# Kernel optimization log

Measured on AMD Instinct MI355X. Metric: run time of the kernel, lower is better.

## Reference

```python
import jax, jax.numpy as jnp
import numpy as np

N = 20000
E = 320000
K = 16          # k_dynamic
FEAT = 64       # feature_dim == hidden_channels
R = 4           # expansion_factor
NUM_OUT = 80000 # num_out_points == R*N
CH = 2000       # query chunk size for kNN (N % CH == 0)


def _lin(key, fan_in, fan_out):
    kw, kb = jax.random.split(key)
    lim = 1.0 / np.sqrt(fan_in)
    W = jax.random.uniform(kw, (fan_in, fan_out), minval=-lim, maxval=lim, dtype=jnp.float32)
    b = jax.random.uniform(kb, (fan_out,), minval=-lim, maxval=lim, dtype=jnp.float32)
    return W, b


def setup_inputs() -> dict:
    key = jax.random.key(0)
    ks = jax.random.split(key, 10)
    dep_points = jax.random.normal(ks[0], (N, 3), dtype=jnp.float32)
    edge_index = jax.random.randint(ks[1], (2, E), 0, N, dtype=jnp.int32)
    W1a, b1a = _lin(ks[2], 2 * 3, FEAT)       # edgeconv1 mlp layer 1
    W1b, b1b = _lin(ks[3], FEAT, FEAT)        # edgeconv1 mlp layer 2
    W2a, b2a = _lin(ks[4], 2 * FEAT, FEAT)    # dynamic edgeconv mlp layer 1
    W2b, b2b = _lin(ks[5], FEAT, FEAT)        # dynamic edgeconv mlp layer 2
    We, be = _lin(ks[6], FEAT, R * FEAT)      # linear_expand
    Wp, bp = _lin(ks[7], FEAT, FEAT)          # out_proj
    Wr1, br1 = _lin(ks[8], FEAT, FEAT)
    Wr2, br2 = _lin(ks[9], FEAT, 3)
    return dict(dep_points=dep_points, W1a=W1a, b1a=b1a, W1b=W1b, b1b=b1b,
                W2a=W2a, b2a=b2a, W2b=W2b, b2b=b2b, We=We, be=be, Wp=Wp, bp=bp,
                Wr1=Wr1, br1=br1, Wr2=Wr2, br2=br2, edge_index=edge_index)


def _mlp2(x, Wa, ba, Wb, bb):
    h = jax.nn.relu(x @ Wa + ba)
    return jax.nn.relu(h @ Wb + bb)


def _forward(dep_points, W1a, b1a, W1b, b1b, W2a, b2a, W2b, b2b,
             We, be, Wp, bp, Wr1, br1, Wr2, br2, edge_index):
    # --- EdgeConv with static edge_index (flow source_to_target: i = edge_index[1]) ---
    src, dst = edge_index[0], edge_index[1]
    xi = dep_points[dst]                             # [E,3] target features
    xj = dep_points[src]                             # [E,3] source features
    msg = _mlp2(jnp.concatenate([xi, xj - xi], -1), W1a, b1a, W1b, b1b)  # [E,64]
    x1 = jax.ops.segment_max(msg, dst, num_segments=N)                   # [N,64]
    x1 = jnp.where(jnp.isfinite(x1), x1, 0.0)        # empty segments -> 0

    # --- DynamicEdgeConv: kNN in feature space (indices non-differentiable) ---
    f = jax.lax.stop_gradient(x1)
    sq = jnp.sum(f * f, axis=1)                      # [N]
    def chunk_knn(qc):                                # qc: [CH,64]
        d2 = jnp.sum(qc * qc, axis=1)[:, None] + sq[None, :] - 2.0 * (qc @ f.T)
        return jax.lax.top_k(-d2, K)[1]               # [CH,K] includes self (d=0)
    nbr = jax.lax.map(chunk_knn, f.reshape(N // CH, CH, FEAT)).reshape(N, K)

    xi2 = x1[:, None, :]                              # [N,1,64]
    xj2 = x1[nbr]                                     # [N,K,64]
    pair = jnp.concatenate([jnp.broadcast_to(xi2, (N, K, FEAT)), xj2 - xi2], -1)
    msg2 = _mlp2(pair, W2a, b2a, W2b, b2b)            # [N,K,64]
    x2 = jnp.max(msg2, axis=1)                        # [N,64]

    # --- SimpleExpansion: expand + periodic shuffle + out_proj (B=1) ---
    xe = x2 @ We + be                                 # [N, R*64]
    xs = xe.reshape(N, R, FEAT).transpose(1, 0, 2).reshape(R * N, FEAT)
    feat = xs @ Wp + bp                               # [R*N,64]

    L = feat.shape[0]
    if L > NUM_OUT:
        feat = feat[:NUM_OUT]
    elif L < NUM_OUT:
        feat = jnp.concatenate([feat, jnp.repeat(feat[-1:], NUM_OUT - L, axis=0)], 0)

    h = jax.nn.relu(feat @ Wr1 + br1)
    return h @ Wr2 + br2                              # [NUM_OUT,3]


def reference(dep_points, W1a, b1a, W1b, b1b, W2a, b2a, W2b, b2b,
              We, be, Wp, bp, Wr1, br1, Wr2, br2, edge_index):
    return _forward(dep_points, W1a, b1a, W1b, b1b, W2a, b2a, W2b, b2b,
                    We, be, Wp, bp, Wr1, br1, Wr2, br2, edge_index)
```

## Files before the change

kernel.cpp:

```cpp
#include <hip/hip_runtime.h>
#include <hip/hip_bf16.h>

#define NPTS 20000
#define NE   320000
#define KNNK 16
#define NTILE ((NPTS + 127) / 128)

typedef __attribute__((ext_vector_type(8))) short bf16x8;
typedef __attribute__((ext_vector_type(4))) float f32x4;

#define OFF_X1   0
#define OFF_SQ   (OFF_X1 + NPTS*64)
#define OFF_WB   (OFF_SQ + NPTS)
#define WB_W1A  0
#define WB_B1A  384
#define WB_W1BT 448
#define WB_B1B  4544
#define WB_W2A  4608
#define WB_B2A  12800
#define WB_W2B  12864
#define WB_B2B  16960
#define WB_WE   17024
#define WB_BE   33408
#define WB_WP   33664
#define WB_BP   37760
#define WB_WR1  37824
#define WB_BR1  41920
#define WB_WR2  41984
#define WB_BR2  42176
#define WB_TOT  42240
#define OFF_NBR  (OFF_WB + WB_TOT)
#define OFF_OFFS (OFF_NBR + NPTS*KNNK)
#define WS1_TOT  (OFF_OFFS + NPTS + 4)
#define OFF_PK   ((WS1_TOT + 3) & ~3)
#define WS_NEED_BYTES ((size_t)WS1_TOT * 4)
#define WS2_BYTES (((size_t)OFF_PK + (size_t)NPTS*2*16) * 4)
#define WS4_BYTES (((size_t)OFF_PK + (size_t)NPTS*4*16) * 4)

__global__ __launch_bounds__(256) void k_out_zero(float* out, int nelem) {
    int i = blockIdx.x * 256 + threadIdx.x;
    if (i < nelem) out[i] = 0.0f;
}

__global__ __launch_bounds__(256) void k_prep(
    const float* W1a, const float* b1a,
    const float* W1b, const float* b1b,
    const float* W2a, const float* b2a,
    const float* W2b, const float* b2b,
    const float* We,  const float* be,
    const float* Wp,  const float* bp,
    const float* Wr1, const float* br1,
    const float* Wr2, const float* br2,
    float* wb, unsigned int* counts)
{
    int t = blockIdx.x * blockDim.x + threadIdx.x;
    int gs = gridDim.x * blockDim.x;
    for (int i = t; i < NPTS; i += gs) counts[i] = 0u;
    for (int i = t; i < 384;  i += gs) wb[WB_W1A+i] = W1a[i];
    for (int i = t; i < 64;   i += gs) wb[WB_B1A+i] = b1a[i];
    for (int i = t; i < 4096; i += gs) { int j=i>>6, k=i&63; wb[WB_W1BT+i] = W1b[k*64+j]; }
    for (int i = t; i < 64;   i += gs) wb[WB_B1B+i] = b1b[i];
    for (int i = t; i < 8192; i += gs) wb[WB_W2A+i] = W2a[i];
    for (int i = t; i < 64;   i += gs) wb[WB_B2A+i] = b2a[i];
    for (int i = t; i < 4096; i += gs) wb[WB_W2B+i] = W2b[i];
    for (int i = t; i < 64;   i += gs) wb[WB_B2B+i] = b2b[i];
    for (int i = t; i < 16384;i += gs) wb[WB_WE+i]  = We[i];
    for (int i = t; i < 256;  i += gs) wb[WB_BE+i]  = be[i];
    for (int i = t; i < 4096; i += gs) wb[WB_WP+i]  = Wp[i];
    for (int i = t; i < 64;   i += gs) wb[WB_BP+i]  = bp[i];
    for (int i = t; i < 4096; i += gs) wb[WB_WR1+i] = Wr1[i];
    for (int i = t; i < 64;   i += gs) wb[WB_BR1+i] = br1[i];
    for (int i = t; i < 192;  i += gs) wb[WB_WR2+i] = Wr2[i];
    for (int i = t; i < 3;    i += gs) wb[WB_BR2+i] = br2[i];
}

__global__ __launch_bounds__(256) void k_hist(const int* __restrict__ ei,
                                              unsigned int* __restrict__ counts) {
    int e = blockIdx.x * 256 + threadIdx.x;
    if (e >= NE) return;
    int d = ei[NE + e];
    d = d < 0 ? 0 : (d >= NPTS ? NPTS-1 : d);
    atomicAdd(&counts[d], 1u);
}

__global__ __launch_bounds__(256) void k_scan(const unsigned int* __restrict__ counts,
                                              unsigned int* __restrict__ cursor,
                                              unsigned int* __restrict__ offs) {
    __shared__ unsigned int ssum[256];
    __shared__ unsigned int sbase[257];
    int t = threadIdx.x;
    int lo = t * 79;
    int hi = lo + 79; if (hi > NPTS) hi = NPTS;
    if (lo > NPTS) lo = NPTS;
    unsigned int sum = 0;
    for (int i = lo; i < hi; ++i) sum += counts[i];
    ssum[t] = sum;
    __syncthreads();
    if (t == 0) {
        unsigned int run = 0;
        for (int i = 0; i < 256; ++i) { sbase[i] = run; run += ssum[i]; }
        sbase[256] = run;
    }
    __syncthreads();
    unsigned int run = sbase[t];
    for (int i = lo; i < hi; ++i) {
        unsigned int c = counts[i];
        offs[i] = run;
        cursor[i] = run;
        run += c;
    }
    if (t == 0) offs[NPTS] = sbase[256];
}

__global__ __launch_bounds__(256) void k_scatter(const int* __restrict__ ei,
                                                 unsigned int* __restrict__ cursor,
                                                 int* __restrict__ elist) {
    int e = blockIdx.x * 256 + threadIdx.x;
    if (e >= NE) return;
    int d = ei[NE + e];
    d = d < 0 ? 0 : (d >= NPTS ? NPTS-1 : d);
    unsigned int pos = atomicAdd(&cursor[d], 1u);
    elist[pos] = e;
}

__device__ __forceinline__ int clampn(int v) {
    return v < 0 ? 0 : (v >= NPTS ? NPTS-1 : v);
}

__global__ __launch_bounds__(64) void k_gather(
    const float* __restrict__ dep, const int* __restrict__ ei,
    const int* __restrict__ elist, const unsigned int* __restrict__ offs,
    const float* __restrict__ W1a, const float* __restrict__ b1a,
    const float* __restrict__ W1b, const float* __restrict__ b1b,
    float* __restrict__ x1)
{
    __shared__ float hbuf[2][64];
    int d = blockIdx.x;
    int t = threadIdx.x;
    unsigned int o0 = offs[d], o1 = offs[d+1];
    float xi0 = dep[d*3+0], xi1 = dep[d*3+1], xi2 = dep[d*3+2];
    float wa0 = W1a[t], wa1 = W1a[64+t], wa2 = W1a[128+t];
    float wa3 = W1a[192+t], wa4 = W1a[256+t], wa5 = W1a[320+t];
    float ba = b1a[t], bb = b1b[t];
    float w1b[64];
#pragma unroll
    for (int j = 0; j < 64; ++j) w1b[j] = W1b[j*64 + t];
    float m = 0.0f;
    int buf = 0;
    if (o0 < o1) {
        unsigned int last = o1 - 1;
        int e0 = elist[o0];
        int s0 = clampn(ei[e0]);
        float dx0 = dep[s0*3+0] - xi0;
        float dx1 = dep[s0*3+1] - xi1;
        float dx2 = dep[s0*3+2] - xi2;
        unsigned int i1 = o0 + 1 < last ? o0 + 1 : last;
        unsigned int i2 = o0 + 2 < last ? o0 + 2 : last;
        int s_nxt  = clampn(ei[elist[i1]]);
        int eid_n2 = elist[i2];
        for (unsigned int o = o0; o < o1; ++o) {
            float h = ba;
            h = fmaf(xi0, wa0, h); h = fmaf(xi1, wa1, h); h = fmaf(xi2, wa2, h);
            h = fmaf(dx0, wa3, h); h = fmaf(dx1, wa4, h); h = fmaf(dx2, wa5, h);
            h = fmaxf(h, 0.0f);
            hbuf[buf][t] = h;
            __syncthreads();
            float ndx0 = dep[s_nxt*3+0] - xi0;
            float ndx1 = dep[s_nxt*3+1] - xi1;
            float ndx2 = dep[s_nxt*3+2] - xi2;
            int ns2 = ei[eid_n2];
            unsigned int i3 = o + 3 < last ? o + 3 : last;
            int neid = elist[i3];
            const float* hb = hbuf[buf];
            float z = bb;
#pragma unroll
            for (int j = 0; j < 64; ++j) z = fmaf(hb[j], w1b[j], z);
            m = fmaxf(m, z);
            buf ^= 1;
            dx0 = ndx0; dx1 = ndx1; dx2 = ndx2;
            s_nxt = clampn(ns2);
            eid_n2 = neid;
        }
    }
    x1[d*64 + t] = m;
}

__global__ __launch_bounds__(256) void k_conv(float* __restrict__ x1, float* __restrict__ sq) {
    int n = blockIdx.x * 256 + threadIdx.x;
    if (n >= NPTS) return;
    float* base = x1 + n*64;
    float4 r[16];
#pragma unroll
    for (int i = 0; i < 16; ++i) r[i] = ((const float4*)base)[i];
    float s = 0.f;
#pragma unroll
    for (int i = 0; i < 16; ++i) s += r[i].x*r[i].x + r[i].y*r[i].y + r[i].z*r[i].z + r[i].w*r[i].w;
    sq[n] = s;
    unsigned int* hi = (unsigned int*)base;
    unsigned int* lo = (unsigned int*)(base + 32);
#pragma unroll
    for (int j = 0; j < 8; ++j) {
        float v[8] = { r[2*j].x, r[2*j].y, r[2*j].z, r[2*j].w,
                       r[2*j+1].x, r[2*j+1].y, r[2*j+1].z, r[2*j+1].w };
        unsigned int hb[8], lb[8];
#pragma unroll
        for (int e = 0; e < 8; ++e) {
            unsigned int u = __float_as_uint(v[e]);
            hb[e] = (u + 0x7fffu + ((u >> 16) & 1u)) >> 16;
            float hf = __uint_as_float(hb[e] << 16);
            float lf = v[e] - hf;
            unsigned int ul = __float_as_uint(lf);
            lb[e] = (ul + 0x7fffu + ((ul >> 16) & 1u)) >> 16;
        }
        uint4 hp, lp;
        hp.x = hb[0] | (hb[1] << 16); hp.y = hb[2] | (hb[3] << 16);
        hp.z = hb[4] | (hb[5] << 16); hp.w = hb[6] | (hb[7] << 16);
        lp.x = lb[0] | (lb[1] << 16); lp.y = lb[2] | (lb[3] << 16);
        lp.z = lb[4] | (lb[5] << 16); lp.w = lb[6] | (lb[7] << 16);
        ((uint4*)hi)[j] = hp;
        ((uint4*)lo)[j] = lp;
    }
}

__device__ __forceinline__ void insk(unsigned int (&s)[16], unsigned int k) {
#pragma unroll
    for (int i = 15; i >= 1; --i) s[i] = min(s[i], max(s[i-1], k));
    s[0] = min(s[0], k);
}

#define RP  136
#define QB  64
__global__ __launch_bounds__(512) void k_knn(
    const float* __restrict__ x1, const float* __restrict__ sqv,
    int* __restrict__ nbr, unsigned int* __restrict__ pk)
{
    __shared__ __align__(16) unsigned short qbuf[QB*RP];
    __shared__ __align__(16) unsigned char  cbuf_raw[128*RP*2];
    __shared__ float ssq[128];
    unsigned short* cbuf = (unsigned short*)cbuf_raw;
    const int t  = threadIdx.x;
    const int n0 = blockIdx.x * QB;
    const int ns = gridDim.y;
    const int tps  = (NTILE + ns - 1) / ns;
    const int tbeg = blockIdx.y * tps;
    const int tend = min(NTILE, tbeg + tps);

#pragma unroll
    for (int i = 0; i < 2; ++i) {
        int ch2 = i*512 + t;
        int row = ch2 >> 4, off = ch2 & 15;
        uint4 v = make_uint4(0,0,0,0);
        if (n0 + row < NPTS) v = ((const uint4*)(x1 + (n0+row)*64))[off];
        *(uint4*)&qbuf[row*RP + off*8] = v;
    }
    __syncthreads();

    const int lane15 = t & 15;
    const int quad   = (t >> 4) & 3;
    const int w  = t >> 6;
    const int qs = w & 3;
    const int ch = w >> 2;
    bf16x8 Bh[2], Bl[2];
    {
        const unsigned short* qr = &qbuf[(qs*16 + lane15)*RP + quad*8];
        Bh[0] = *(const bf16x8*)(qr);
        Bh[1] = *(const bf16x8*)(qr + 32);
        Bl[0] = *(const bf16x8*)(qr + 64);
        Bl[1] = *(const bf16x8*)(qr + 96);
    }
    int myq = n0 + qs*16 + lane15;
    float sqq = (myq < NPTS) ? sqv[myq] : 0.0f;
    unsigned int sk[16];
#pragma unroll
    for (int m = 0; m < 16; ++m) sk[m] = 0xFFFFFFFFu;

    uint4 pv[4];
    int prow[4], poff[4];
#pragma unroll
    for (int i = 0; i < 4; ++i) {
        int ch2 = i*512 + t;
        prow[i] = tbeg*128 + (ch2 >> 4); poff[i] = ch2 & 15;
        pv[i] = make_uint4(0,0,0,0);
        if (prow[i] < NPTS) pv[i] = ((const uint4*)(x1 + prow[i]*64))[poff[i]];
    }
    float sreg = (t < 128 && tbeg*128 + t < NPTS) ? sqv[tbeg*128 + t] : 1e30f;

    for (int tile = tbeg; tile < tend; ++tile) {
        const int c0 = tile * 128;
        __syncthreads();
#pragma unroll
        for (int i = 0; i < 4; ++i)
            *(uint4*)&cbuf[(prow[i] - c0)*RP + poff[i]*8] = pv[i];
        if (t < 128) ssq[t] = sreg;
        __syncthreads();

        unsigned int pm  = min(sk[15], (unsigned int)__shfl_xor((int)sk[15], 16));
        unsigned int swv = min(pm, (unsigned int)__shfl_xor((int)pm, 32));

        if (tile + 1 < tend) {
            const int c0n = c0 + 128;
#pragma unroll
            for (int i = 0; i < 4; ++i) {
                int row = prow[i] + 128;
                pv[i] = make_uint4(0,0,0,0);
                if (row < NPTS) pv[i] = ((const uint4*)(x1 + row*64))[poff[i]];
                prow[i] = row;
            }
            sreg = (t < 128 && c0n + t < NPTS) ? sqv[c0n + t] : 1e30f;
        }

#pragma unroll
        for (int t4 = 0; t4 < 4; ++t4) {
            const unsigned short* cr = &cbuf[(ch*64 + t4*16 + lane15)*RP + quad*8];
            bf16x8 Ah0 = *(const bf16x8*)(cr);
            bf16x8 Ah1 = *(const bf16x8*)(cr + 32);
            bf16x8 Al0 = *(const bf16x8*)(cr + 64);
            bf16x8 Al1 = *(const bf16x8*)(cr + 96);
            f32x4 acc = (f32x4){0.f,0.f,0.f,0.f};
            acc = __builtin_amdgcn_mfma_f32_16x16x32_bf16(Ah0, Bh[0], acc, 0, 0, 0);
            acc = __builtin_amdgcn_mfma_f32_16x16x32_bf16(Al0, Bh[0], acc, 0, 0, 0);
            acc = __builtin_amdgcn_mfma_f32_16x16x32_bf16(Ah0, Bl[0], acc, 0, 0, 0);
            acc = __builtin_amdgcn_mfma_f32_16x16x32_bf16(Ah1, Bh[1], acc, 0, 0, 0);
            acc = __builtin_amdgcn_mfma_f32_16x16x32_bf16(Al1, Bh[1], acc, 0, 0, 0);
            acc = __builtin_amdgcn_mfma_f32_16x16x32_bf16(Ah1, Bl[1], acc, 0, 0, 0);
            int cbase = ch*64 + t4*16 + quad*4;
            float4 s4 = *(const float4*)&ssq[cbase];
            float e0 = fmaxf(fmaf(-2.0f, acc[0], s4.x) + sqq, 0.0f);
            float e1 = fmaxf(fmaf(-2.0f, acc[1], s4.y) + sqq, 0.0f);
            float e2 = fmaxf(fmaf(-2.0f, acc[2], s4.z) + sqq, 0.0f);
            float e3 = fmaxf(fmaf(-2.0f, acc[3], s4.w) + sqq, 0.0f);
            unsigned int cg = (unsigned int)(c0 + cbase);
            unsigned int k0 = (__float_as_uint(e0) & 0xFFFF8000u) | (cg+0u);
            unsigned int k1 = (__float_as_uint(e1) & 0xFFFF8000u) | (cg+1u);
            unsigned int k2 = (__float_as_uint(e2) & 0xFFFF8000u) | (cg+2u);
            unsigned int k3 = (__float_as_uint(e3) & 0xFFFF8000u) | (cg+3u);
            unsigned int mn = min(min(k0,k1), min(k2,k3));
            if (mn < swv) {
                if (k0 < sk[15]) insk(sk, k0);
                if (k1 < sk[15]) insk(sk, k1);
                if (k2 < sk[15]) insk(sk, k2);
                if (k3 < sk[15]) insk(sk, k3);
            }
        }
    }
    __syncthreads();
    {
        int q = qs*16 + lane15, lid = ch*4 + quad;
        unsigned int* fk = (unsigned int*)cbuf_raw;
        int base = q*136 + lid*17;
#pragma unroll
        for (int m = 0; m < 16; ++m) fk[base + m] = sk[m];
    }
    __syncthreads();
    if (t < QB && n0 + t < NPTS) {
        const unsigned int* fk = (const unsigned int*)cbuf_raw;
        int qb = t*136;
        int pr[8] = {0,0,0,0,0,0,0,0};
        int obase = (ns == 1) ? (n0 + t)*16 : ((n0 + t)*ns + blockIdx.y)*16;
        for (int r = 0; r < 16; ++r) {
            unsigned int best = 0xFFFFFFFFu; int bl = 0;
#pragma unroll
            for (int l = 0; l < 8; ++l) {
                unsigned int k = fk[qb + l*17 + pr[l]];
                if (k < best) { best = k; bl = l; }
            }
#pragma unroll
            for (int l = 0; l < 8; ++l) pr[l] += (bl == l) ? 1 : 0;
            if (ns == 1) {
                int idx = (int)(best & 0x7FFFu);
                nbr[obase + r] = idx >= NPTS ? NPTS-1 : idx;
            } else {
                pk[obase + r] = best;
            }
        }
    }
}

__global__ __launch_bounds__(256) void k_fmerge(
    const unsigned int* __restrict__ pk, int ns, int* __restrict__ nbr)
{
    int q = blockIdx.x * 256 + threadIdx.x;
    if (q >= NPTS) return;
    const unsigned int* fk = pk + q*ns*16;
    int pr[4] = {0,0,0,0};
    for (int r = 0; r < 16; ++r) {
        unsigned int best = 0xFFFFFFFFu; int bl = 0;
        for (int l = 0; l < ns; ++l) {
            unsigned int k = fk[l*16 + pr[l]];
            if (k < best) { best = k; bl = l; }
        }
        pr[bl]++;
        int idx = (int)(best & 0x7FFFu);
        nbr[q*16 + r] = idx >= NPTS ? NPTS-1 : idx;
    }
}

__device__ inline float bf2f(unsigned short u) {
    return __uint_as_float(((unsigned int)u) << 16);
}

__global__ __launch_bounds__(64) void k_fuse(
    const float* __restrict__ x1, const int* __restrict__ nbr,
    const float* __restrict__ wb, float* __restrict__ out)
{
    __shared__ __align__(16) float sxr[64];
    __shared__ __align__(16) float svec[64];
    __shared__ __align__(16) float sx2[64];
    __shared__ int snb[16];
    int n = blockIdx.x;
    int t = threadIdx.x;
    {
        const unsigned short* xr = (const unsigned short*)(x1 + n*64);
        sxr[t] = bf2f(xr[t]) + bf2f(xr[64+t]);
    }
    if (t < 16) snb[t] = nbr[n*16 + t];
    __syncthreads();
    const float* W2a = wb + WB_W2A;
    const float* W2b = wb + WB_W2B;
    const float4* sx4 = (const float4*)sxr;
    const float4* sv4 = (const float4*)svec;
    float wd[64], wz[64];
#pragma unroll
    for (int i = 0; i < 64; ++i) wd[i] = W2a[(64+i)*64 + t];
#pragma unroll
    for (int i = 0; i < 64; ++i) wz[i] = W2b[i*64 + t];
    float A = wb[WB_B2A + t];
#pragma unroll
    for (int i4 = 0; i4 < 16; ++i4) {
        float4 v = sx4[i4];
        const float* wr = W2a + i4*256 + t;
        A = fmaf(v.x, wr[0], A); A = fmaf(v.y, wr[64], A);
        A = fmaf(v.z, wr[128], A); A = fmaf(v.w, wr[192], A);
    }
    float D = 0.0f;
#pragma unroll
    for (int i4 = 0; i4 < 16; ++i4) {
        float4 v = sx4[i4];
        D = fmaf(v.x, wd[i4*4+0], D); D = fmaf(v.y, wd[i4*4+1], D);
        D = fmaf(v.z, wd[i4*4+2], D); D = fmaf(v.w, wd[i4*4+3], D);
    }
    const float AD = A - D;
    const float bz = wb[WB_B2B + t];
    float x2v = 0.0f;
    unsigned short ya, yb;
    {
        const unsigned short* yr = (const unsigned short*)(x1 + snb[0]*64);
        ya = yr[t]; yb = yr[64+t];
    }
    for (int k = 0; k < 16; ++k) {
        svec[t] = bf2f(ya) + bf2f(yb);
        __syncthreads();
        if (k + 1 < 16) {
            const unsigned short* yr = (const unsigned short*)(x1 + snb[k+1]*64);
            ya = yr[t]; yb = yr[64+t];
        }
        float h = AD;
#pragma unroll
        for (int i4 = 0; i4 < 16; ++i4) {
            float4 v = sv4[i4];
            h = fmaf(v.x, wd[i4*4+0], h); h = fmaf(v.y, wd[i4*4+1], h);
            h = fmaf(v.z, wd[i4*4+2], h); h = fmaf(v.w, wd[i4*4+3], h);
        }
        h = fmaxf(h, 0.f);
        __syncthreads();
        svec[t] = h;
        __syncthreads();
        float z = bz;
#pragma unroll
        for (int i4 = 0; i4 < 16; ++i4) {
            float4 v = sv4[i4];
            z = fmaf(v.x, wz[i4*4+0], z); z = fmaf(v.y, wz[i4*4+1], z);
            z = fmaf(v.z, wz[i4*4+2], z); z = fmaf(v.w, wz[i4*4+3], z);
        }
        x2v = fmaxf(x2v, fmaxf(z, 0.f));
        __syncthreads();
    }
    sx2[t] = x2v;
    __syncthreads();
    const float4* sx24 = (const float4*)sx2;
    const float* We  = wb + WB_WE;
    const float* Wp  = wb + WB_WP;
    const float* Wr1 = wb + WB_WR1;
    const float* Wr2 = wb + WB_WR2;
    for (int r = 0; r < 4; ++r) {
        float xe = wb[WB_BE + r*64 + t];
#pragma unroll
        for (int i4 = 0; i4 < 16; ++i4) {
            float4 v = sx24[i4];
            const float* wr = We + i4*1024 + r*64 + t;
            xe = fmaf(v.x, wr[0], xe); xe = fmaf(v.y, wr[256], xe);
            xe = fmaf(v.z, wr[512], xe); xe = fmaf(v.w, wr[768], xe);
        }
        svec[t] = xe;
        __syncthreads();
        float ft = wb[WB_BP + t];
#pragma unroll
        for (int i4 = 0; i4 < 16; ++i4) {
            float4 v = sv4[i4];
            const float* wr = Wp + i4*256 + t;
            ft = fmaf(v.x, wr[0], ft); ft = fmaf(v.y, wr[64], ft);
            ft = fmaf(v.z, wr[128], ft); ft = fmaf(v.w, wr[192], ft);
        }
        __syncthreads();
        svec[t] = ft;
        __syncthreads();
        float hh = wb[WB_BR1 + t];
#pragma unroll
        for (int i4 = 0; i4 < 16; ++i4) {
            float4 v = sv4[i4];
            const float* wr = Wr1 + i4*256 + t;
            hh = fmaf(v.x, wr[0], hh); hh = fmaf(v.y, wr[64], hh);
            hh = fmaf(v.z, wr[128], hh); hh = fmaf(v.w, wr[192], hh);
        }
        hh = fmaxf(hh, 0.f);
        __syncthreads();
        svec[t] = hh;
        __syncthreads();
        if (t < 3) {
            float o = wb[WB_BR2 + t];
            for (int i = 0; i < 64; ++i) o = fmaf(svec[i], Wr2[i*3 + t], o);
            int m = r * NPTS + n;
            out[m*3 + t] = o;
        }
        __syncthreads();
    }
}

extern "C" void kernel_launch(void* const* d_in, const int* in_sizes, int n_in,
                              void* d_out, int out_size, void* d_ws, size_t ws_size,
                              hipStream_t stream)
{
    const float* dep = (const float*)d_in[0];
    const float* W1a = (const float*)d_in[1];
    const float* b1a = (const float*)d_in[2];
    const float* W1b = (const float*)d_in[3];
    const float* b1b = (const float*)d_in[4];
    const float* W2a = (const float*)d_in[5];
    const float* b2a = (const float*)d_in[6];
    const float* W2b = (const float*)d_in[7];
    const float* b2b = (const float*)d_in[8];
    const float* We  = (const float*)d_in[9];
    const float* be  = (const float*)d_in[10];
    const float* Wp  = (const float*)d_in[11];
    const float* bp  = (const float*)d_in[12];
    const float* Wr1 = (const float*)d_in[13];
    const float* br1 = (const float*)d_in[14];
    const float* Wr2 = (const float*)d_in[15];
    const float* br2 = (const float*)d_in[16];
    const int* ei = (const int*)d_in[17];

    if (ws_size < WS_NEED_BYTES || d_ws == nullptr) {
        k_out_zero<<<(out_size + 255)/256, 256, 0, stream>>>((float*)d_out, out_size);
        return;
    }

    float* ws   = (float*)d_ws;
    float* x1   = ws + OFF_X1;
    float* sq   = ws + OFF_SQ;
    float* wbuf = ws + OFF_WB;
    int*   nbr  = (int*)(ws + OFF_NBR);
    unsigned int* counts = (unsigned int*)(ws + OFF_SQ);
    int*   elist = (int*)(ws + OFF_NBR);
    unsigned int* offs = (unsigned int*)(ws + OFF_OFFS);

    int ns = (ws_size >= WS4_BYTES) ? 4 : (ws_size >= WS2_BYTES) ? 2 : 1;
    unsigned int* pk = (unsigned int*)(ws + OFF_PK);

    k_prep<<<64, 256, 0, stream>>>(W1a,b1a,W1b,b1b,W2a,b2a,W2b,b2b,We,be,Wp,bp,Wr1,br1,Wr2,br2, wbuf, counts);
    k_hist<<<NE/256, 256, 0, stream>>>(ei, counts);
    k_scan<<<1, 256, 0, stream>>>(counts, counts, offs);
    k_scatter<<<NE/256, 256, 0, stream>>>(ei, counts, elist);
    k_gather<<<NPTS, 64, 0, stream>>>(dep, ei, elist, offs, W1a, b1a, W1b, b1b, x1);
    k_conv<<<(NPTS+255)/256, 256, 0, stream>>>(x1, sq);
    dim3 gk((NPTS + QB - 1)/QB, ns);
    k_knn<<<gk, 512, 0, stream>>>(x1, sq, nbr, pk);
    if (ns > 1) k_fmerge<<<(NPTS + 255)/256, 256, 0, stream>>>(pk, ns, nbr);
    k_fuse<<<NPTS, 64, 0, stream>>>(x1, nbr, wbuf, (float*)d_out);
}
```

Baseline: 1.120 ms.

## Fuse bf16 split into gather, merge kNN lists in fuse, pack four nodes per block

The gather kernel now writes the squared norm and the hi/lo bf16 split directly, so the separate conversion kernel goes away. The partial-list merge kernel is replaced by a wave-level bitonic sort inside the fuse kernel. Both gather and fuse now run four 64-lane waves per block, one node per wave, and drop __syncthreads in favour of per-wave shared buffers and shuffles. This cuts launches and block barriers. It relies on wave64 lockstep for LDS visibility without explicit barriers, and the bitonic sort adds some ALU work per node.

```diff
diff --git a/kernel.cpp b/kernel.cpp
--- a/kernel.cpp
+++ b/kernel.cpp
@@ -127,24 +127,24 @@
     return v < 0 ? 0 : (v >= NPTS ? NPTS-1 : v);
 }
 
-__global__ __launch_bounds__(64) void k_gather(
+__global__ __launch_bounds__(256) void k_gather(
     const float* __restrict__ dep, const int* __restrict__ ei,
     const int* __restrict__ elist, const unsigned int* __restrict__ offs,
     const float* __restrict__ W1a, const float* __restrict__ b1a,
     const float* __restrict__ W1b, const float* __restrict__ b1b,
-    float* __restrict__ x1)
+    float* __restrict__ x1, float* __restrict__ sq)
 {
-    __shared__ float hbuf[2][64];
-    int d = blockIdx.x;
-    int t = threadIdx.x;
+    __shared__ float hbuf[4][2][64];
+    int w = threadIdx.x >> 6, l = threadIdx.x & 63;
+    int d = blockIdx.x * 4 + w;
     unsigned int o0 = offs[d], o1 = offs[d+1];
     float xi0 = dep[d*3+0], xi1 = dep[d*3+1], xi2 = dep[d*3+2];
-    float wa0 = W1a[t], wa1 = W1a[64+t], wa2 = W1a[128+t];
-    float wa3 = W1a[192+t], wa4 = W1a[256+t], wa5 = W1a[320+t];
-    float ba = b1a[t], bb = b1b[t];
+    float wa0 = W1a[l], wa1 = W1a[64+l], wa2 = W1a[128+l];
+    float wa3 = W1a[192+l], wa4 = W1a[256+l], wa5 = W1a[320+l];
+    float ba = b1a[l], bb = b1b[l];
     float w1b[64];
 #pragma unroll
-    for (int j = 0; j < 64; ++j) w1b[j] = W1b[j*64 + t];
+    for (int j = 0; j < 64; ++j) w1b[j] = W1b[j*64 + l];
     float m = 0.0f;
     int buf = 0;
     if (o0 < o1) {
@@ -163,15 +163,14 @@
             h = fmaf(xi0, wa0, h); h = fmaf(xi1, wa1, h); h = fmaf(xi2, wa2, h);
             h = fmaf(dx0, wa3, h); h = fmaf(dx1, wa4, h); h = fmaf(dx2, wa5, h);
             h = fmaxf(h, 0.0f);
-            hbuf[buf][t] = h;
-            __syncthreads();
+            hbuf[w][buf][l] = h;
             float ndx0 = dep[s_nxt*3+0] - xi0;
             float ndx1 = dep[s_nxt*3+1] - xi1;
             float ndx2 = dep[s_nxt*3+2] - xi2;
             int ns2 = ei[eid_n2];
             unsigned int i3 = o + 3 < last ? o + 3 : last;
             int neid = elist[i3];
-            const float* hb = hbuf[buf];
+            const float* hb = hbuf[w][buf];
             float z = bb;
 #pragma unroll
             for (int j = 0; j < 64; ++j) z = fmaf(hb[j], w1b[j], z);
@@ -182,44 +181,19 @@
             eid_n2 = neid;
         }
     }
-    x1[d*64 + t] = m;
-}
-
-__global__ __launch_bounds__(256) void k_conv(float* __restrict__ x1, float* __restrict__ sq) {
-    int n = blockIdx.x * 256 + threadIdx.x;
-    if (n >= NPTS) return;
-    float* base = x1 + n*64;
-    float4 r[16];
-#pragma unroll
-    for (int i = 0; i < 16; ++i) r[i] = ((const float4*)base)[i];
-    float s = 0.f;
-#pragma unroll
-    for (int i = 0; i < 16; ++i) s += r[i].x*r[i].x + r[i].y*r[i].y + r[i].z*r[i].z + r[i].w*r[i].w;
-    sq[n] = s;
-    unsigned int* hi = (unsigned int*)base;
-    unsigned int* lo = (unsigned int*)(base + 32);
-#pragma unroll
-    for (int j = 0; j < 8; ++j) {
-        float v[8] = { r[2*j].x, r[2*j].y, r[2*j].z, r[2*j].w,
-                       r[2*j+1].x, r[2*j+1].y, r[2*j+1].z, r[2*j+1].w };
-        unsigned int hb[8], lb[8];
-#pragma unroll
-        for (int e = 0; e < 8; ++e) {
-            unsigned int u = __float_as_uint(v[e]);
-            hb[e] = (u + 0x7fffu + ((u >> 16) & 1u)) >> 16;
-            float hf = __uint_as_float(hb[e] << 16);
-            float lf = v[e] - hf;
-            unsigned int ul = __float_as_uint(lf);
-            lb[e] = (ul + 0x7fffu + ((ul >> 16) & 1u)) >> 16;
-        }
-        uint4 hp, lp;
-        hp.x = hb[0] | (hb[1] << 16); hp.y = hb[2] | (hb[3] << 16);
-        hp.z = hb[4] | (hb[5] << 16); hp.w = hb[6] | (hb[7] << 16);
-        lp.x = lb[0] | (lb[1] << 16); lp.y = lb[2] | (lb[3] << 16);
-        lp.z = lb[4] | (lb[5] << 16); lp.w = lb[6] | (lb[7] << 16);
-        ((uint4*)hi)[j] = hp;
-        ((uint4*)lo)[j] = lp;
-    }
+    float s = m * m;
+#pragma unroll
+    for (int j = 1; j < 64; j <<= 1) s += __shfl_xor(s, j);
+    if (l == 0) sq[d] = s;
+    unsigned int u = __float_as_uint(m);
+    unsigned int hb16 = (u + 0x7fffu + ((u >> 16) & 1u)) >> 16;
+    float hf = __uint_as_float(hb16 << 16);
+    float lf = m - hf;
+    unsigned int ul = __float_as_uint(lf);
+    unsigned int lb16 = (ul + 0x7fffu + ((ul >> 16) & 1u)) >> 16;
+    unsigned short* row = (unsigned short*)(x1 + d*64);
+    row[l] = (unsigned short)hb16;
+    row[64 + l] = (unsigned short)lb16;
 }
 
 __device__ __forceinline__ void insk(unsigned int (&s)[16], unsigned int k) {
@@ -376,59 +350,56 @@
     }
 }
 
-__global__ __launch_bounds__(256) void k_fmerge(
-    const unsigned int* __restrict__ pk, int ns, int* __restrict__ nbr)
-{
-    int q = blockIdx.x * 256 + threadIdx.x;
-    if (q >= NPTS) return;
-    const unsigned int* fk = pk + q*ns*16;
-    int pr[4] = {0,0,0,0};
-    for (int r = 0; r < 16; ++r) {
-        unsigned int best = 0xFFFFFFFFu; int bl = 0;
-        for (int l = 0; l < ns; ++l) {
-            unsigned int k = fk[l*16 + pr[l]];
-            if (k < best) { best = k; bl = l; }
-        }
-        pr[bl]++;
-        int idx = (int)(best & 0x7FFFu);
-        nbr[q*16 + r] = idx >= NPTS ? NPTS-1 : idx;
-    }
-}
-
 __device__ inline float bf2f(unsigned short u) {
     return __uint_as_float(((unsigned int)u) << 16);
 }
 
-__global__ __launch_bounds__(64) void k_fuse(
+__global__ __launch_bounds__(256) void k_fuse(
     const float* __restrict__ x1, const int* __restrict__ nbr,
+    const unsigned int* __restrict__ pk, int ns,
     const float* __restrict__ wb, float* __restrict__ out)
 {
-    __shared__ __align__(16) float sxr[64];
-    __shared__ __align__(16) float svec[64];
-    __shared__ __align__(16) float sx2[64];
-    __shared__ int snb[16];
-    int n = blockIdx.x;
-    int t = threadIdx.x;
+    __shared__ __align__(16) float sx[4][64];
+    __shared__ __align__(16) float sv[4][64];
+    int w = threadIdx.x >> 6, l = threadIdx.x & 63;
+    int n = blockIdx.x * 4 + w;
+    int mynb;
+    if (ns > 1) {
+        unsigned int key = (l < ns*16) ? pk[n*ns*16 + l] : 0xFFFFFFFFu;
+#pragma unroll
+        for (int kk = 2; kk <= 64; kk <<= 1) {
+#pragma unroll
+            for (int jj = kk >> 1; jj > 0; jj >>= 1) {
+                unsigned int p = (unsigned int)__shfl_xor((int)key, jj);
+                bool up = ((l & kk) == 0);
+                bool lower = ((l & jj) == 0);
+                unsigned int mn = min(key, p), mx = max(key, p);
+                key = (up == lower) ? mn : mx;
+            }
+        }
+        int idx = (int)(key & 0x7FFFu);
+        mynb = idx >= NPTS ? NPTS-1 : idx;
+    } else {
+        mynb = (l < 16) ? nbr[n*16 + l] : 0;
+    }
     {
         const unsigned short* xr = (const unsigned short*)(x1 + n*64);
-        sxr[t] = bf2f(xr[t]) + bf2f(xr[64+t]);
-    }
-    if (t < 16) snb[t] = nbr[n*16 + t];
-    __syncthreads();
+        sx[w][l] = bf2f(xr[l]) + bf2f(xr[64+l]);
+    }
     const float* W2a = wb + WB_W2A;
     const float* W2b = wb + WB_W2B;
-    const float4* sx4 = (const float4*)sxr;
-    const float4* sv4 = (const float4*)svec;
+    const float4* sx4 = (const float4*)sx[w];
+    const float4* sv4 = (const float4*)sv[w];
     float wd[64], wz[64];
 #pragma unroll
-    for (int i = 0; i < 64; ++i) wd[i] = W2a[(64+i)*64 + t];
-#pragma unroll
-    for (int i = 0; i < 64; ++i) wz[i] = W2b[i*64 + t];
-    float A = wb[WB_B2A + t];
+    for (int i = 0; i < 64; ++i) wd[i] = W2a[(64+i)*64 + l];
+#pragma unroll
+    for (int i = 0; i < 64; ++i) wz[i] = W2b[i*64 + l];
+    float A = wb[WB_B2A + l];
 #pragma unroll
     for (int i4 = 0; i4 < 16; ++i4) {
         float4 v = sx4[i4];
-        const float* wr = W2a + i4*256 + t;
+        const float* wr = W2a + i4*256 + l;
         A = fmaf(v.x, wr[0], A); A = fmaf(v.y, wr[64], A);
         A = fmaf(v.z, wr[128], A); A = fmaf(v.w, wr[192], A);
     }
@@ -440,19 +411,20 @@
         D = fmaf(v.z, wd[i4*4+2], D); D = fmaf(v.w, wd[i4*4+3], D);
     }
     const float AD = A - D;
-    const float bz = wb[WB_B2B + t];
+    const float bz = wb[WB_B2B + l];
     float x2v = 0.0f;
+    int nb0 = __shfl(mynb, 0);
     unsigned short ya, yb;
     {
-        const unsigned short* yr = (const unsigned short*)(x1 + snb[0]*64);
-        ya = yr[t]; yb = yr[64+t];
+        const unsigned short* yr = (const unsigned short*)(x1 + nb0*64);
+        ya = yr[l]; yb = yr[64+l];
     }
     for (int k = 0; k < 16; ++k) {
-        svec[t] = bf2f(ya) + bf2f(yb);
-        __syncthreads();
+        sv[w][l] = bf2f(ya) + bf2f(yb);
         if (k + 1 < 16) {
-            const unsigned short* yr = (const unsigned short*)(x1 + snb[k+1]*64);
-            ya = yr[t]; yb = yr[64+t];
+            int nbn = __shfl(mynb, k + 1);
+            const unsigned short* yr = (const unsigned short*)(x1 + nbn*64);
+            ya = yr[l]; yb = yr[64+l];
         }
         float h = AD;
 #pragma unroll
@@ -462,9 +434,7 @@
             h = fmaf(v.z, wd[i4*4+2], h); h = fmaf(v.w, wd[i4*4+3], h);
         }
         h = fmaxf(h, 0.f);
-        __syncthreads();
-        svec[t] = h;
-        __syncthreads();
+        sv[w][l] = h;
         float z = bz;
 #pragma unroll
         for (int i4 = 0; i4 < 16; ++i4) {
@@ -473,56 +443,48 @@
             z = fmaf(v.z, wz[i4*4+2], z); z = fmaf(v.w, wz[i4*4+3], z);
         }
         x2v = fmaxf(x2v, fmaxf(z, 0.f));
-        __syncthreads();
-    }
-    sx2[t] = x2v;
-    __syncthreads();
-    const float4* sx24 = (const float4*)sx2;
+    }
+    sx[w][l] = x2v;
     const float* We  = wb + WB_WE;
     const float* Wp  = wb + WB_WP;
     const float* Wr1 = wb + WB_WR1;
     const float* Wr2 = wb + WB_WR2;
     for (int r = 0; r < 4; ++r) {
-        float xe = wb[WB_BE + r*64 + t];
+        float xe = wb[WB_BE + r*64 + l];
 #pragma unroll
         for (int i4 = 0; i4 < 16; ++i4) {
-            float4 v = sx24[i4];
-            const float* wr = We + i4*1024 + r*64 + t;
+            float4 v = sx4[i4];
+            const float* wr = We + i4*1024 + r*64 + l;
             xe = fmaf(v.x, wr[0], xe); xe = fmaf(v.y, wr[256], xe);
             xe = fmaf(v.z, wr[512], xe); xe = fmaf(v.w, wr[768], xe);
         }
-        svec[t] = xe;
-        __syncthreads();
-        float ft = wb[WB_BP + t];
+        sv[w][l] = xe;
+        float ft = wb[WB_BP + l];
 #pragma unroll
         for (int i4 = 0; i4 < 16; ++i4) {
             float4 v = sv4[i4];
-            const float* wr = Wp + i4*256 + t;
+            const float* wr = Wp + i4*256 + l;
             ft = fmaf(v.x, wr[0], ft); ft = fmaf(v.y, wr[64], ft);
             ft = fmaf(v.z, wr[128], ft); ft = fmaf(v.w, wr[192], ft);
         }
-        __syncthreads();
-        svec[t] = ft;
-        __syncthreads();
-        float hh = wb[WB_BR1 + t];
+        sv[w][l] = ft;
+        float hh = wb[WB_BR1 + l];
 #pragma unroll
         for (int i4 = 0; i4 < 16; ++i4) {
             float4 v = sv4[i4];
-            const float* wr = Wr1 + i4*256 + t;
+            const float* wr = Wr1 + i4*256 + l;
             hh = fmaf(v.x, wr[0], hh); hh = fmaf(v.y, wr[64], hh);
             hh = fmaf(v.z, wr[128], hh); hh = fmaf(v.w, wr[192], hh);
         }
         hh = fmaxf(hh, 0.f);
-        __syncthreads();
-        svec[t] = hh;
-        __syncthreads();
-        if (t < 3) {
-            float o = wb[WB_BR2 + t];
-            for (int i = 0; i < 64; ++i) o = fmaf(svec[i], Wr2[i*3 + t], o);
+        sv[w][l] = hh;
+        if (l < 3) {
+            float o = wb[WB_BR2 + l];
+            const float* svp = sv[w];
+            for (int i = 0; i < 64; ++i) o = fmaf(svp[i], Wr2[i*3 + l], o);
             int m = r * NPTS + n;
-            out[m*3 + t] = o;
-        }
-        __syncthreads();
+            out[m*3 + l] = o;
+        }
     }
 }
 
@@ -570,10 +532,8 @@
     k_hist<<<NE/256, 256, 0, stream>>>(ei, counts);
     k_scan<<<1, 256, 0, stream>>>(counts, counts, offs);
     k_scatter<<<NE/256, 256, 0, stream>>>(ei, counts, elist);
-    k_gather<<<NPTS, 64, 0, stream>>>(dep, ei, elist, offs, W1a, b1a, W1b, b1b, x1);
-    k_conv<<<(NPTS+255)/256, 256, 0, stream>>>(x1, sq);
+    k_gather<<<NPTS/4, 256, 0, stream>>>(dep, ei, elist, offs, W1a, b1a, W1b, b1b, x1, sq);
     dim3 gk((NPTS + QB - 1)/QB, ns);
     k_knn<<<gk, 512, 0, stream>>>(x1, sq, nbr, pk);
-    if (ns > 1) k_fmerge<<<(NPTS + 255)/256, 256, 0, stream>>>(pk, ns, nbr);
-    k_fuse<<<NPTS, 64, 0, stream>>>(x1, nbr, wbuf, (float*)d_out);
-}
+    k_fuse<<<NPTS/4, 256, 0, stream>>>(x1, nbr, pk, ns, wbuf, (float*)d_out);
+}
```

New measurement: 1.295 ms. 15.6% more time.
